# Kernel optimization log

Measured on AMD Instinct MI355X. Metric: run time of the kernel, lower is better.

## Reference

```python
import jax, jax.numpy as jnp
import numpy as np

B, S, E, H, C = 2, 2048, 1024, 16, 16
SQ2 = np.float32(np.sqrt(2.0))


def setup_inputs() -> dict:
    key = jax.random.key(0)
    ks = jax.random.split(key, 32)
    sc = 0.02
    d = {"query": jax.random.normal(ks[0], (B, S, E), jnp.float32)}
    i = 1
    for dom in ("f", "w", "c"):
        d[f"Wp_{dom}"] = jax.random.normal(ks[i], (E, E), jnp.float32) * sc; i += 1
        d[f"bp_{dom}"] = jnp.zeros((E,), jnp.float32)
        d[f"Wc_{dom}"] = jax.random.normal(ks[i], (C, E, 3), jnp.float32) * sc; i += 1
        d[f"bc_{dom}"] = jnp.zeros((C,), jnp.float32)
        d["F" + dom] = jax.random.normal(ks[i], (C, E), jnp.float32); i += 1
    d["mha_iw"] = jax.random.normal(ks[i], (3 * E, E), jnp.float32) * sc; i += 1
    d["mha_ib"] = jnp.zeros((3 * E,), jnp.float32)
    d["mha_ow"] = jax.random.normal(ks[i], (E, E), jnp.float32) * sc; i += 1
    d["mha_ob"] = jnp.zeros((E,), jnp.float32)
    d["fus_W"] = jax.random.normal(ks[i], (E, 3 * E), jnp.float32) * sc; i += 1
    d["fus_b"] = jnp.zeros((E,), jnp.float32)
    return d


def _conv1d(x, W, b):
    # x: [B,S,E] real -> [B,S,C], conv over sequence, kernel 3, same padding
    y = jax.lax.conv_general_dilated(x.transpose(0, 2, 1), W, (1,), [(1, 1)],
                                     dimension_numbers=("NCH", "OIH", "NCH"))
    return (y + b[None, :, None]).transpose(0, 2, 1)


def _channels(x, Wc, bc, Fp):
    # spectral conv (real/imag separately if complex) + adaptive softmax filtering
    if jnp.iscomplexobj(x):
        ch = _conv1d(x.real, Wc, bc) + 1j * _conv1d(x.imag, Wc, bc)
    else:
        ch = _conv1d(x, Wc, bc)
    fw = jax.nn.softmax(Fp, axis=0)  # [C,E], softmax over channels
    return jnp.einsum("bsc,ce->bse", ch, fw.astype(ch.dtype))


def _spec_attn(q, k, v):
    scale = np.float32(1.0) / jnp.sqrt(jnp.asarray(q.shape[-1], jnp.float32))
    scores = jnp.einsum("bse,bte->bst", q, k) * scale
    if jnp.iscomplexobj(scores):
        w = jax.nn.softmax(scores.real, axis=-1)
        cw = (w * jnp.exp(1j * jnp.angle(scores))).astype(jnp.complex64)
        return jnp.einsum("bst,bte->bse", cw, v)
    return jnp.einsum("bst,bte->bse", jax.nn.softmax(scores, axis=-1), v)


def _haar(x):
    # simplified Haar wavelet transform; S is a power of 2 so no padding needed
    cur, coeffs = x, []
    while cur.shape[1] > 1:
        e, o = cur[:, 0::2, :], cur[:, 1::2, :]
        coeffs.append((e - o) / SQ2)
        cur = (e + o) / SQ2
    coeffs.append(cur)
    return jnp.concatenate(coeffs[::-1], axis=1)


def _dct_mats(L):
    n = jnp.arange(L, dtype=jnp.float32)
    k = n[:, None]
    D = jnp.cos(np.pi * k * (2.0 * n + 1.0) / (2.0 * L))
    D = D.at[0].multiply(np.float32(np.sqrt(1.0 / L)))
    D = D.at[1:].multiply(np.float32(np.sqrt(2.0 / L)))
    I = jnp.cos(np.pi * n * (2.0 * k + 1.0) / (2.0 * L))
    I = I.at[:, 0].multiply(np.float32(np.sqrt(1.0 / L)))
    I = I.at[:, 1:].multiply(np.float32(np.sqrt(2.0 / L)))
    return D, I


def _domain(x, Wp, bp, Wc, bc, Fp, domain):
    # key=value=query so q_domain == k_domain == v_domain
    xd = x @ Wp.T + bp
    if domain == "fourier":
        s = jnp.fft.fft(xd, axis=1)
        ch = _channels(s, Wc, bc, Fp)
        out = _spec_attn(ch, ch, ch)
        return jnp.fft.ifft(out, axis=1).real
    elif domain == "wavelet":
        s = _haar(xd)
        ch = _channels(s, Wc, bc, Fp)
        return _spec_attn(ch, ch, ch)  # inverse wavelet is identity in source
    else:  # cosine
        D, I = _dct_mats(xd.shape[1])
        s = jnp.einsum("st,bte->bse", D, xd)
        ch = _channels(s, Wc, bc, Fp)
        out = _spec_attn(ch, ch, ch)
        return jnp.einsum("st,bte->bse", I, out)


def _mha(x, iw, ib, ow, ob, nheads):
    # torch nn.MultiheadAttention (batch_first) self-attention
    Bx, L, Ex = x.shape
    hd = Ex // nheads
    qkv = x @ iw.T + ib
    q, k, v = jnp.split(qkv, 3, axis=-1)
    sh = lambda t: t.reshape(Bx, L, nheads, hd).transpose(0, 2, 1, 3)
    q, k, v = sh(q), sh(k), sh(v)
    a = jax.nn.softmax(jnp.einsum("bhld,bhmd->bhlm", q, k) / np.float32(np.sqrt(hd)), axis=-1)
    o = jnp.einsum("bhlm,bhmd->bhld", a, v).transpose(0, 2, 1, 3).reshape(Bx, L, Ex)
    return o @ ow.T + ob


def reference(query, Wp_f, bp_f, Wc_f, bc_f, Ff, Wp_w, bp_w, Wc_w, bc_w, Fw,
              Wp_c, bp_c, Wc_c, bc_c, Fc, mha_iw, mha_ib, mha_ow, mha_ob, fus_W, fus_b):
    outs = [
        _domain(query, Wp_f, bp_f, Wc_f, bc_f, Ff, "fourier"),
        _domain(query, Wp_w, bp_w, Wc_w, bc_w, Fw, "wavelet"),
        _domain(query, Wp_c, bp_c, Wc_c, bc_c, Fc, "cosine"),
    ]
    Bq, Sq, Eq = query.shape
    stacked = jnp.stack(outs, axis=2)                 # [B,S,3,E]
    corr = _mha(stacked.reshape(Bq * Sq, 3, Eq), mha_iw, mha_ib, mha_ow, mha_ob, H)
    fused = corr.reshape(Bq, Sq, 3 * Eq)              # concat of correlated domain outputs
    return fused @ fus_W.T + fus_b
```

## Files before the change

### kernel.cpp

```cpp
#include <hip/hip_runtime.h>
#include <cmath>

#define BB 2
#define SS_ 2048
#define EE 1024
#define CC 16

typedef __attribute__((ext_vector_type(8))) short short8v;
typedef __attribute__((ext_vector_type(4))) float floatx4;

__device__ __forceinline__ void split4(const float4 v, short4& h, short4& l)
{
    unsigned ux = __float_as_uint(v.x), uy = __float_as_uint(v.y);
    unsigned uz = __float_as_uint(v.z), uw = __float_as_uint(v.w);
    h.x = (short)(ux >> 16); h.y = (short)(uy >> 16);
    h.z = (short)(uz >> 16); h.w = (short)(uw >> 16);
    float lx = v.x - __uint_as_float(ux & 0xFFFF0000u);
    float ly = v.y - __uint_as_float(uy & 0xFFFF0000u);
    float lz = v.z - __uint_as_float(uz & 0xFFFF0000u);
    float lw = v.w - __uint_as_float(uw & 0xFFFF0000u);
    l.x = (short)(__float_as_uint(lx) >> 16);
    l.y = (short)(__float_as_uint(ly) >> 16);
    l.z = (short)(__float_as_uint(lz) >> 16);
    l.w = (short)(__float_as_uint(lw) >> 16);
}

#define BM 128
#define BN 128
#define BK 32
#define LDP 40

__launch_bounds__(256, 2)
__global__ void gemm_at(const float* __restrict__ A, const float* __restrict__ Bsrc,
                        float* __restrict__ C,
                        int K, int lda, int ldb, int ldc,
                        long sA, long sB, long sC, float alpha, int KS)
{
    __shared__ short sAh[BM * LDP], sAl[BM * LDP], sBh[BN * LDP], sBl[BN * LDP];
    const int z = blockIdx.z;
    const int bz = z / KS, ks = z % KS;
    const int klen = K / KS, kbase = ks * klen;
    A += (size_t)bz * sA; Bsrc += (size_t)bz * sB; C += (size_t)bz * sC;
    const int tid = threadIdx.x;
    const int m0 = blockIdx.y * BM, n0 = blockIdx.x * BN;

    const int lr0 = tid >> 3;
    const int kc0 = (tid & 7) * 4;
    const float* pa = A + (size_t)(m0 + lr0) * lda + kbase + kc0;
    const float* pb = Bsrc + (size_t)(n0 + lr0) * ldb + kbase + kc0;

    float4 ra[4], rb[4];
    #pragma unroll
    for (int c = 0; c < 4; ++c) {
        ra[c] = *(const float4*)(pa + (size_t)c * 32 * lda);
        rb[c] = *(const float4*)(pb + (size_t)c * 32 * ldb);
    }

    const int lane = tid & 63, wid = tid >> 6;
    const int wm = wid >> 1, wn = wid & 1;
    const int lr = lane & 15, qd = lane >> 4;
    const int arow = wm * 64 + lr;
    const int brow = wn * 64 + lr;
    const int koff = qd * 8;

    floatx4 acc[4][4];
    #pragma unroll
    for (int i = 0; i < 4; ++i)
        #pragma unroll
        for (int j = 0; j < 4; ++j)
            acc[i][j] = (floatx4){0.f, 0.f, 0.f, 0.f};

    for (int kt = 0; kt < klen; kt += BK) {
        __syncthreads();
        #pragma unroll
        for (int c = 0; c < 4; ++c) {
            const int row = lr0 + c * 32;
            short4 h, l;
            split4(ra[c], h, l);
            *(short4*)&sAh[row * LDP + kc0] = h;
            *(short4*)&sAl[row * LDP + kc0] = l;
            split4(rb[c], h, l);
            *(short4*)&sBh[row * LDP + kc0] = h;
            *(short4*)&sBl[row * LDP + kc0] = l;
        }
        __syncthreads();
        if (kt + BK < klen) {
            pa += BK; pb += BK;
            #pragma unroll
            for (int c = 0; c < 4; ++c) {
                ra[c] = *(const float4*)(pa + (size_t)c * 32 * lda);
                rb[c] = *(const float4*)(pb + (size_t)c * 32 * ldb);
            }
        }
        short8v ah[4], al[4], bh[4], bl[4];
        #pragma unroll
        for (int i = 0; i < 4; ++i) {
            ah[i] = *(const short8v*)&sAh[(arow + i * 16) * LDP + koff];
            al[i] = *(const short8v*)&sAl[(arow + i * 16) * LDP + koff];
            bh[i] = *(const short8v*)&sBh[(brow + i * 16) * LDP + koff];
            bl[i] = *(const short8v*)&sBl[(brow + i * 16) * LDP + koff];
        }
        #pragma unroll
        for (int i = 0; i < 4; ++i)
            #pragma unroll
            for (int j = 0; j < 4; ++j)
                acc[i][j] = __builtin_amdgcn_mfma_f32_16x16x32_bf16(ah[i], bh[j], acc[i][j], 0, 0, 0);
        #pragma unroll
// ... 359 lines not shown

__launch_bounds__(256)
__global__ void conv_all(const float* __restrict__ Tfr, const float* __restrict__ Tfi,
                         const float* __restrict__ Tw, const float* __restrict__ Tc,
                         const float* __restrict__ Gm,
                         const float* __restrict__ bc0, const float* __restrict__ bc1,
                         const float* __restrict__ bc2,
                         float* __restrict__ chFr, float* __restrict__ chFi,
                         float* __restrict__ chW, float* __restrict__ chC,
                         float* __restrict__ QFr, float* __restrict__ QFi,
                         float* __restrict__ QW, float* __restrict__ QC)
{
    const int dom = blockIdx.z;
    const bool cplx = (dom == 0);
    const float* Tre = dom == 0 ? Tfr : (dom == 1 ? Tw : Tc);
    const float* Tim = Tfi;
    const float* G = Gm + dom * 256;
    const float* bc = dom == 0 ? bc0 : (dom == 1 ? bc1 : bc2);
    float* chR = dom == 0 ? chFr : (dom == 1 ? chW : chC);
    float* chI = chFi;
    float* QR = dom == 0 ? QFr : (dom == 1 ? QW : QC);
    float* QI = QFi;

    const int s0 = blockIdx.x * 64, b = blockIdx.y;
    const int tid = threadIdx.x;
    __shared__ float sR[66 * 49];
    __shared__ float sI[66 * 49];
    __shared__ float scr[64 * 17];
    __shared__ float sci[64 * 17];
    __shared__ float sG[256];
    if (tid < 256) sG[tid] = G[tid];
    for (int lin = tid; lin < 66 * 12; lin += 256) {
        int r = lin / 12, c4 = (lin % 12) * 4;
        int srow = s0 - 1 + r;
        float4 v = {0.f, 0.f, 0.f, 0.f}, w = {0.f, 0.f, 0.f, 0.f};
        if (srow >= 0 && srow < 2048) {
            v = *(const float4*)(Tre + ((size_t)(b * 2048 + srow)) * 48 + c4);
            if (cplx) w = *(const float4*)(Tim + ((size_t)(b * 2048 + srow)) * 48 + c4);
        }
        sR[r * 49 + c4] = v.x; sR[r * 49 + c4 + 1] = v.y;
        sR[r * 49 + c4 + 2] = v.z; sR[r * 49 + c4 + 3] = v.w;
        if (cplx) {
            sI[r * 49 + c4] = w.x; sI[r * 49 + c4 + 1] = w.y;
            sI[r * 49 + c4 + 2] = w.z; sI[r * 49 + c4 + 3] = w.w;
        }
    }
    __syncthreads();
    const int row = tid >> 2, ln = tid & 3;
    float ch[4], chi[4];
    #pragma unroll
    for (int j = 0; j < 4; ++j) {
        int c = ln * 4 + j;
        float bcv = bc[c];
        ch[j] = sR[row * 49 + 3 * c] + sR[(row + 1) * 49 + 3 * c + 1]
              + sR[(row + 2) * 49 + 3 * c + 2] + bcv;
        scr[row * 17 + c] = ch[j];
        if (cplx) {
            chi[j] = sI[row * 49 + 3 * c] + sI[(row + 1) * 49 + 3 * c + 1]
                   + sI[(row + 2) * 49 + 3 * c + 2] + bcv;
            sci[row * 17 + c] = chi[j];
        }
    }
    size_t ro = ((size_t)(b * 2048 + s0 + row)) * 16 + ln * 4;
    *(float4*)(chR + ro) = *(float4*)&ch[0];
    if (cplx) *(float4*)(chI + ro) = *(float4*)&chi[0];
    __syncthreads();
    float qp[4] = {}, qpi[4] = {};
    #pragma unroll
    for (int c = 0; c < 16; ++c) {
        float cv = scr[row * 17 + c];
        float cvi = cplx ? sci[row * 17 + c] : 0.f;
        #pragma unroll
        for (int j = 0; j < 4; ++j) {
            float g = sG[c * 16 + ln * 4 + j];
            qp[j] = fmaf(cv, g, qp[j]);
            if (cplx) qpi[j] = fmaf(cvi, g, qpi[j]);
        }
    }
    *(float4*)(QR + ro) = *(float4*)&qp[0];
    if (cplx) *(float4*)(QI + ro) = *(float4*)&qpi[0];
}

__launch_bounds__(256)
__global__ void flash_all(const float* __restrict__ QpFr, const float* __restrict__ QpFi,
                          const float* __restrict__ chFr, const float* __restrict__ chFi,
                          float* __restrict__ OFr, float* __restrict__ OFi,
                          const float* __restrict__ QpW, const float* __restrict__ chW,
                          float* __restrict__ Ow_,
                          const float* __restrict__ QpC, const float* __restrict__ chC,
                          float* __restrict__ Oc_)
{
    const int dom = blockIdx.z;
    const int b = blockIdx.y;
    const int w = threadIdx.x >> 6, lane = threadIdx.x & 63;
    const int s = blockIdx.x * 4 + w;
    if (dom != 0) {
        const float* Qp = dom == 1 ? QpW : QpC;
        const float* ch = dom == 1 ? chW : chC;
        float* O = dom == 1 ? Ow_ : Oc_;
        const float* qrow = Qp + ((size_t)(b * 2048 + s)) * 16;
        float q[16];
        #pragma unroll
        for (int j = 0; j < 4; ++j) *(float4*)&q[j * 4] = *(const float4*)(qrow + j * 4);
        const float* chb = ch + (size_t)b * 2048 * 16;
        float m = -3.4e38f, l = 0.f;
        float acc[16] = {};
        for (int t = lane; t < 2048; t += 64) {
            const float* kp = chb + (size_t)t * 16;
            float kv[16];
            #pragma unroll
            for (int j = 0; j < 4; ++j) *(float4*)&kv[j * 4] = *(const float4*)(kp + j * 4);
            float sc = 0.f;
            #pragma unroll
            for (int e = 0; e < 16; ++e) sc = fmaf(q[e], kv[e], sc);
            float mn = fmaxf(m, sc);
            float al = __expf(m - mn), p = __expf(sc - mn);
            l = l * al + p;
            #pragma unroll
            for (int e = 0; e < 16; ++e) acc[e] = fmaf(acc[e], al, p * kv[e]);
            m = mn;
        }
        #pragma unroll
        for (int off = 1; off < 64; off <<= 1) {
            float m2 = __shfl_xor(m, off, 64);
            float l2 = __shfl_xor(l, off, 64);
            float mn = fmaxf(m, m2);
            float ra = __expf(m - mn), rb = __expf(m2 - mn);
            l = l * ra + l2 * rb;
            #pragma unroll
            for (int e = 0; e < 16; ++e) {
                float a2 = __shfl_xor(acc[e], off, 64);
                acc[e] = acc[e] * ra + a2 * rb;
            }
            m = mn;
        }
        if (lane < 4) {
            float inv = 1.f / l;
            float4 o4 = {acc[lane * 4] * inv, acc[lane * 4 + 1] * inv,
                         acc[lane * 4 + 2] * inv, acc[lane * 4 + 3] * inv};
            *(float4*)(O + ((size_t)(b * 2048 + s)) * 16 + lane * 4) = o4;
        }
        return;
    }
    float qr[16], qi[16];
    {
        const float* qrow = QpFr + ((size_t)(b * 2048 + s)) * 16;
        const float* qrowI = QpFi + ((size_t)(b * 2048 + s)) * 16;
        #pragma unroll
        for (int j = 0; j < 4; ++j) {
            *(float4*)&qr[j * 4] = *(const float4*)(qrow + j * 4);
            *(float4*)&qi[j * 4] = *(const float4*)(qrowI + j * 4);
        }
    }
    const float* cbR = chFr + (size_t)b * 2048 * 16;
    const float* cbI = chFi + (size_t)b * 2048 * 16;
    float m = -3.4e38f, l = 0.f;
    float aR[16] = {}, aI[16] = {};
    for (int t = lane; t < 2048; t += 64) {
        float kr[16], ki[16];
        #pragma unroll
        for (int j = 0; j < 4; ++j) {
            *(float4*)&kr[j * 4] = *(const float4*)(cbR + (size_t)t * 16 + j * 4);
            *(float4*)&ki[j * 4] = *(const float4*)(cbI + (size_t)t * 16 + j * 4);
        }
        float sre = 0.f, sim = 0.f;
        #pragma unroll
        for (int e = 0; e < 16; ++e) {
            sre = fmaf(qr[e], kr[e], sre); sre = fmaf(-qi[e], ki[e], sre);
            sim = fmaf(qr[e], ki[e], sim); sim = fmaf(qi[e], kr[e], sim);
        }
        float mn = fmaxf(m, sre);
        float al = __expf(m - mn), p = __expf(sre - mn);
        l = l * al + p;
        float rr = sqrtf(sre * sre + sim * sim);
        float iv = (rr > 0.f) ? (p / rr) : 0.f;
        float wr = (rr > 0.f) ? iv * sre : p;
        float wi = (rr > 0.f) ? iv * sim : 0.f;
        #pragma unroll
        for (int e = 0; e < 16; ++e) {
            aR[e] = fmaf(aR[e], al, wr * kr[e] - wi * ki[e]);
            aI[e] = fmaf(aI[e], al, wr * ki[e] + wi * kr[e]);
        }
        m = mn;
    }
    #pragma unroll
    for (int off = 1; off < 64; off <<= 1) {
        float m2 = __shfl_xor(m, off, 64);
        float l2 = __shfl_xor(l, off, 64);
        float mn = fmaxf(m, m2);
        float ra = __expf(m - mn), rb = __expf(m2 - mn);
        l = l * ra + l2 * rb;
        #pragma unroll
        for (int e = 0; e < 16; ++e) {
            float a2 = __shfl_xor(aR[e], off, 64);
            aR[e] = aR[e] * ra + a2 * rb;
            float b2 = __shfl_xor(aI[e], off, 64);
            aI[e] = aI[e] * ra + b2 * rb;
        }
        m = mn;
    }
    float inv = 1.f / l;
    size_t ro = ((size_t)(b * 2048 + s)) * 16;
    if (lane < 4) {
        float4 o4 = {aR[lane * 4] * inv, aR[lane * 4 + 1] * inv,
                     aR[lane * 4 + 2] * inv, aR[lane * 4 + 3] * inv};
        *(float4*)(OFr + ro + lane * 4) = o4;
    } else if (lane < 8) {
        int j = lane - 4;
        float4 o4 = {aI[j * 4] * inv, aI[j * 4 + 1] * inv,
                     aI[j * 4 + 2] * inv, aI[j * 4 + 3] * inv};
        *(float4*)(OFi + ro + j * 4) = o4;
    }
}

__launch_bounds__(256)
__global__ void mha_o(const float* __restrict__ R0, const float* __restrict__ R1,
                      const float* __restrict__ R2, const float* __restrict__ Pt,
                      const float* __restrict__ Mten, float* __restrict__ MO)
{
    const int tid = threadIdx.x;
    const int p = blockIdx.x * 256 + tid;
    const int h = blockIdx.y;
    __shared__ float sPv[3 * 64 * 20];
    __shared__ float sM[9 * 17 * 20];
    for (int lin = tid; lin < 3264; lin += 256) {
        int mm = lin / 1088, rem = lin % 1088;
        int rr = rem / 17, a = rem % 17;
        sPv[(mm * 64 + rr) * 20 + a] = Pt[mm * 52224 + (size_t)(2048 + h * 64 + rr) * 17 + a];
    }
    for (int lin = tid; lin < 2601; lin += 256) {
        int lm = lin / 289, rem = lin % 289;
        int a = rem / 17, bq = rem % 17;
        sM[lm * 340 + a * 20 + bq] = Mten[(size_t)h * 2601 + lin];
    }
    __syncthreads();
    float R[3][16];
    float4 R4[3][4];
    #pragma unroll
    for (int j = 0; j < 4; ++j) {
        R4[0][j] = *(const float4*)(R0 + (size_t)p * 16 + j * 4);
        R4[1][j] = *(const float4*)(R1 + (size_t)p * 16 + j * 4);
        R4[2][j] = *(const float4*)(R2 + (size_t)p * 16 + j * 4);
        *(float4*)&R[0][j * 4] = R4[0][j];
        *(float4*)&R[1][j * 4] = R4[1][j];
        *(float4*)&R[2][j * 4] = R4[2][j];
    }
    float w[3][3];
    #pragma unroll
    for (int l = 0; l < 3; ++l) {
        float sc[3];
        #pragma unroll
        for (int mm = 0; mm < 3; ++mm) {
            const float* Mp = &sM[(l * 3 + mm) * 340];
            float s = 0.f;
            #pragma unroll
            for (int a = 0; a < 17; ++a) {
                const float* mr = Mp + a * 20;
                float4 m0 = *(const float4*)(mr), m1 = *(const float4*)(mr + 4);
                float4 m2 = *(const float4*)(mr + 8), m3 = *(const float4*)(mr + 12);
                float t = mr[16];
                t = fmaf(m0.x, R4[mm][0].x, t); t = fmaf(m0.y, R4[mm][0].y, t);
                t = fmaf(m0.z, R4[mm][0].z, t); t = fmaf(m0.w, R4[mm][0].w, t);
                t = fmaf(m1.x, R4[mm][1].x, t); t = fmaf(m1.y, R4[mm][1].y, t);
                t = fmaf(m1.z, R4[mm][1].z, t); t = fmaf(m1.w, R4[mm][1].w, t);
                t = fmaf(m2.x, R4[mm][2].x, t); t = fmaf(m2.y, R4[mm][2].y, t);
                t = fmaf(m2.z, R4[mm][2].z, t); t = fmaf(m2.w, R4[mm][2].w, t);
                t = fmaf(m3.x, R4[mm][3].x, t); t = fmaf(m3.y, R4[mm][3].y, t);
                t = fmaf(m3.z, R4[mm][3].z, t); t = fmaf(m3.w, R4[mm][3].w, t);
                float ra = (a < 16) ? R[l][a] : 1.f;
                s = fmaf(ra, t, s);
            }
            sc[mm] = s;
        }
        float mx = fmaxf(sc[0], fmaxf(sc[1], sc[2]));
        float e0 = expf(sc[0] - mx), e1 = expf(sc[1] - mx), e2 = expf(sc[2] - mx);
        float inv = 1.f / (e0 + e1 + e2);
        w[l][0] = e0 * inv; w[l][1] = e1 * inv; w[l][2] = e2 * inv;
    }
    #pragma unroll
    for (int d4 = 0; d4 < 16; ++d4) {
        float4 vm[3];
        #pragma unroll
        for (int mm = 0; mm < 3; ++mm) {
            float vx[4];
            #pragma unroll
            for (int r = 0; r < 4; ++r) {
                const float* pv = &sPv[(mm * 64 + d4 * 4 + r) * 20];
                float4 p0 = *(const float4*)(pv), p1 = *(const float4*)(pv + 4);
                float4 p2 = *(const float4*)(pv + 8), p3 = *(const float4*)(pv + 12);
                float t = pv[16];
                t = fmaf(R4[mm][0].x, p0.x, t); t = fmaf(R4[mm][0].y, p0.y, t);
                t = fmaf(R4[mm][0].z, p0.z, t); t = fmaf(R4[mm][0].w, p0.w, t);
                t = fmaf(R4[mm][1].x, p1.x, t); t = fmaf(R4[mm][1].y, p1.y, t);
                t = fmaf(R4[mm][1].z, p1.z, t); t = fmaf(R4[mm][1].w, p1.w, t);
                t = fmaf(R4[mm][2].x, p2.x, t); t = fmaf(R4[mm][2].y, p2.y, t);
                t = fmaf(R4[mm][2].z, p2.z, t); t = fmaf(R4[mm][2].w, p2.w, t);
                t = fmaf(R4[mm][3].x, p3.x, t); t = fmaf(R4[mm][3].y, p3.y, t);
                t = fmaf(R4[mm][3].z, p3.z, t); t = fmaf(R4[mm][3].w, p3.w, t);
                vx[r] = t;
            }
            vm[mm] = (float4){vx[0], vx[1], vx[2], vx[3]};
        }
        #pragma unroll
        for (int l = 0; l < 3; ++l) {
            float4 o4;
            o4.x = w[l][0] * vm[0].x + w[l][1] * vm[1].x + w[l][2] * vm[2].x;
            o4.y = w[l][0] * vm[0].y + w[l][1] * vm[1].y + w[l][2] * vm[2].y;
            o4.z = w[l][0] * vm[0].z + w[l][1] * vm[1].z + w[l][2] * vm[2].z;
            o4.w = w[l][0] * vm[0].w + w[l][1] * vm[1].w + w[l][2] * vm[2].w;
            *(float4*)(MO + (size_t)p * 3072 + l * 1024 + h * 64 + d4 * 4) = o4;
        }
    }
}

extern "C" void kernel_launch(void* const* d_in, const int* in_sizes, int n_in,
                              void* d_out, int out_size, void* d_ws, size_t ws_size,
                              hipStream_t stream)
{
    const float* query = (const float*)d_in[0];
    const float* Wp[3] = {(const float*)d_in[1], (const float*)d_in[6],  (const float*)d_in[11]};
    const float* bp[3] = {(const float*)d_in[2], (const float*)d_in[7],  (const float*)d_in[12]};
    const float* Wc[3] = {(const float*)d_in[3], (const float*)d_in[8],  (const float*)d_in[13]};
    const float* bc[3] = {(const float*)d_in[4], (const float*)d_in[9],  (const float*)d_in[14]};
    const float* Fp[3] = {(const float*)d_in[5], (const float*)d_in[10], (const float*)d_in[15]};
    const float* mha_iw = (const float*)d_in[16];
    const float* mha_ib = (const float*)d_in[17];
    const float* mha_ow = (const float*)d_in[18];
    const float* mha_ob = (const float*)d_in[19];
    const float* fus_W  = (const float*)d_in[20];
    const float* fus_b  = (const float*)d_in[21];
    float* out = (float*)d_out;
    float* ws = (float*)d_ws;

    size_t off = 0;
    auto alloc = [&](size_t n) { float* p = ws + off; off += n; return p; };
    float* MAT0 = alloc(4194304);
    float* MAT1 = alloc(4194304);
    float* DCTD = alloc(4194304);
    float* DCTI = alloc(4194304);
    float* MO   = alloc((size_t)4096 * 3072);
    float* FTb  = alloc((size_t)1024 * 3072);
    float* OWT  = alloc((size_t)1024 * 1024);
    float* WpT  = alloc(3145728);
    float* fwT  = alloc(49152);
    float* W2cat = alloc(147456);
    float* ubv  = alloc(256);
    float* Gm   = alloc(1024);
    float* W3cat = alloc(147456);
    float* Ucat = alloc(589824);
    float* Tfr  = alloc(196608);
    float* Tfi  = alloc(196608);
    float* Tc   = alloc(196608);
    float* Rf   = alloc(65536);
    float* Rc   = alloc(65536);
    float* Tw   = alloc(196608);
    float* chFr = alloc(65536); float* chFi = alloc(65536);
    float* QpFr = alloc(65536); float* QpFi = alloc(65536);
    float* chW  = alloc(65536); float* QpW  = alloc(65536);
    float* chC  = alloc(65536); float* QpC  = alloc(65536);
    float* OFr  = alloc(65536); float* OFi  = alloc(65536);
    float* Ow   = alloc(65536); float* Oc   = alloc(65536);
    float* Pt   = alloc(156672);
    float* Mten = alloc(41616);
    float* ybv  = alloc(1024);
    if (ws_size < off * sizeof(float)) return;

    float* Uf = Ucat, *Uw = Ucat + 196608, *Uc = Ucat + 2 * 196608;
    const long SE48 = 2048 * 48, SE16 = 2048 * 16;

    build_w2<<<dim3(576), dim3(256), 0, stream>>>(Wc[0], Wc[1], Wc[2], W2cat);
    prep_fw_G<<<dim3(3), dim3(256), 0, stream>>>(Fp[0], Fp[1], Fp[2], fwT, Gm);
    build_ub2<<<dim3(3), dim3(256), 0, stream>>>(bp[0], bp[1], bp[2], W2cat, ubv);
    build_yb2<<<dim3(256), dim3(256), 0, stream>>>(mha_ob, fus_W, fus_b, ybv);
    gen_trig<<<dim3(32768), dim3(256), 0, stream>>>(MAT0, MAT1, DCTD, DCTI);
    transpose_wp3<<<dim3(32, 32, 3), dim3(256), 0, stream>>>(Wp[0], Wp[1], Wp[2], WpT);
    init_all<<<dim3(34980), dim3(256), 0, stream>>>(W3cat, ubv, Pt, FTb, out, ybv);

    skmfma<48, 0><<<dim3(16, 1, 6), dim3(256), 0, stream>>>(
        WpT, nullptr, W2cat, nullptr, W3cat, nullptr,
        1024, 1024, 48, 48, 1048576, 49152, 49152, 1.f, 2);
    skmfma<48, 0><<<dim3(64, 1, 6), dim3(256), 0, stream>>>(
        query, nullptr, W3cat, nullptr, Ucat, nullptr,
        1024, 1024, 48, 48, 0, 49152, 196608, 1.f, 2);
    skmfma<48, 1><<<dim3(32, 1, 8), dim3(256), 0, stream>>>(
        MAT0, MAT1, Uf, nullptr, Tfr, Tfi,
        2048, 2048, 48, 48, 0, SE48, SE48, 1.f, 4);
    skmfma<48, 0><<<dim3(32, 1, 8), dim3(256), 0, stream>>>(
        DCTD, nullptr, Uc, nullptr, Tc, nullptr,
        2048, 2048, 48, 48, 0, SE48, SE48, 1.f, 4);

    haar_all<<<dim3(12, 2), dim3(256), 0, stream>>>(Uw, Tw);

    conv_all<<<dim3(32, 2, 3), dim3(256), 0, stream>>>(
        Tfr, Tfi, Tw, Tc, Gm, bc[0], bc[1], bc[2],
        chFr, chFi, chW, chC, QpFr, QpFi, QpW, QpC);

    flash_all<<<dim3(512, 2, 3), dim3(256), 0, stream>>>(
        QpFr, QpFi, chFr, chFi, OFr, OFi, QpW, chW, Ow, QpC, chC, Oc);

    skmfma<16, 2><<<dim3(32, 1, 8), dim3(256), 0, stream>>>(
        MAT0, MAT1, OFr, OFi, Rf, nullptr,
        2048, 2048, 16, 16, 0, SE16, SE16, 1.f / 2048.f, 4);
    skmfma<16, 0><<<dim3(32, 1, 8), dim3(256), 0, stream>>>(
        DCTI, nullptr, Oc, nullptr, Rc, nullptr,
        2048, 2048, 16, 16, 0, SE16, SE16, 1.f, 4);
    skmfma<16, 0><<<dim3(48, 1, 6), dim3(256), 0, stream>>>(
        mha_iw, nullptr, fwT, nullptr, Pt, nullptr,
        1024, 1024, 16, 17, 0, 16384, 52224, 1.f, 2);

    ib_append<<<dim3(36), dim3(256), 0, stream>>>(mha_ib, Pt);
    build_M<<<dim3(144), dim3(256), 0, stream>>>(Pt, Mten);

    mha_o<<<dim3(16, 16), dim3(256), 0, stream>>>(Rf, Ow, Rc, Pt, Mten, MO);

    transpose_k<<<dim3(32, 32), dim3(256), 0, stream>>>(mha_ow, OWT, 1024, 1024);
    gemm_at<<<dim3(8, 8, 6), dim3(256), 0, stream>>>(
        fus_W, OWT, FTb, 1024, 3072, 1024, 3072, 1024, 0, 1024, 1.f, 2);

    gemm_at<<<dim3(8, 32, 2), dim3(256), 0, stream>>>(
        MO, FTb, out, 3072, 3072, 3072, 1024, 0, 0, 0, 1.f, 2);
}
```

Measured before the change: 758.5 us.

## Move spectral flash attention onto bf16x3 MFMA with two-pass split-K softmax

Replaces the scalar per-lane online-softmax attention over the 16-wide channel space with an MFMA path. A prep kernel splits Q, K and V into bf16 hi/mid/lo pieces (complex parts arranged for real/imag products), a stats pass computes row max and sum across 4 K-splits, a merge kernel combines them, and a PV pass recomputes scores, forms the weights and accumulates with bf16 split MFMAs plus atomics. This aims to cut the large FMA and exp cost of the fp32 scalar loop. The price is recomputing QK twice, extra launches and scratch traffic (reusing the WpT region), atomic accumulation, and a possible loss of precision from bf16 splitting.

```diff
diff --git a/kernel.cpp b/kernel.cpp
--- a/kernel.cpp
+++ b/kernel.cpp
@@ -23,6 +23,63 @@
     l.y = (short)(__float_as_uint(ly) >> 16);
     l.z = (short)(__float_as_uint(lz) >> 16);
     l.w = (short)(__float_as_uint(lw) >> 16);
+}
+
+__device__ __forceinline__ void split1(float v, short& h, short& l)
+{
+    unsigned u = __float_as_uint(v);
+    h = (short)(u >> 16);
+    float rm = v - __uint_as_float(u & 0xFFFF0000u);
+    l = (short)(__float_as_uint(rm) >> 16);
+}
+
+__device__ __forceinline__ void split4s(float a, float b, float c, float d,
+                                        short4& h, short4& l)
+{
+    split1(a, h.x, l.x); split1(b, h.y, l.y);
+    split1(c, h.z, l.z); split1(d, h.w, l.w);
+}
+
+__device__ __forceinline__ void split3_1(float v, short& x1, short& x2, short& x3)
+{
+    unsigned u = __float_as_uint(v);
+    x1 = (short)(u >> 16);
+    float r1 = v - __uint_as_float(u & 0xFFFF0000u);
+    unsigned u2 = __float_as_uint(r1);
+    x2 = (short)(u2 >> 16);
+    float r2 = r1 - __uint_as_float(u2 & 0xFFFF0000u);
+    x3 = (short)(__float_as_uint(r2) >> 16);
+}
+
+__device__ __forceinline__ void split3s(float a, float b, float c, float d,
+                                        short4& h1, short4& h2, short4& h3)
+{
+    split3_1(a, h1.x, h2.x, h3.x); split3_1(b, h1.y, h2.y, h3.y);
+    split3_1(c, h1.z, h2.z, h3.z); split3_1(d, h1.w, h2.w, h3.w);
+}
+
+__device__ __forceinline__ short4 neg4(short4 a)
+{
+    short4 r;
+    r.x = (short)(a.x ^ (short)0x8000); r.y = (short)(a.y ^ (short)0x8000);
+    r.z = (short)(a.z ^ (short)0x8000); r.w = (short)(a.w ^ (short)0x8000);
+    return r;
+}
+
+__device__ __forceinline__ short8v pack8(short4 a, short4 b)
+{
+    short8v r;
+    r[0] = a.x; r[1] = a.y; r[2] = a.z; r[3] = a.w;
+    r[4] = b.x; r[5] = b.y; r[6] = b.z; r[7] = b.w;
+    return r;
+}
+
+__device__ __forceinline__ short8v negbf(short8v x)
+{
+    int4 t = *(int4*)&x;
+    t.x ^= 0x80008000; t.y ^= 0x80008000;
+    t.z ^= 0x80008000; t.w ^= 0x80008000;
+    return *(short8v*)&t;
 }
 
 #define BM 128
@@ -548,134 +605,378 @@
 }
 
 __launch_bounds__(256)
-__global__ void flash_all(const float* __restrict__ QpFr, const float* __restrict__ QpFi,
-                          const float* __restrict__ chFr, const float* __restrict__ chFi,
-                          float* __restrict__ OFr, float* __restrict__ OFi,
-                          const float* __restrict__ QpW, const float* __restrict__ chW,
-                          float* __restrict__ Ow_,
-                          const float* __restrict__ QpC, const float* __restrict__ chC,
-                          float* __restrict__ Oc_)
-{
-    const int dom = blockIdx.z;
-    const int b = blockIdx.y;
-    const int w = threadIdx.x >> 6, lane = threadIdx.x & 63;
-    const int s = blockIdx.x * 4 + w;
+__global__ void prep_flash(const float* __restrict__ QpFr, const float* __restrict__ QpFi,
+                           const float* __restrict__ chFr, const float* __restrict__ chFi,
+                           const float* __restrict__ QpW, const float* __restrict__ chW,
+                           const float* __restrict__ QpC, const float* __restrict__ chC,
+                           short* __restrict__ AqF, short* __restrict__ BreF,
+                           short* __restrict__ BimF,
+                           short* __restrict__ VtFrH, short* __restrict__ VtFrL,
+                           short* __restrict__ VtFiH, short* __restrict__ VtFiL,
+                           short* __restrict__ AqW, short* __restrict__ KsW,
+                           short* __restrict__ VtWH, short* __restrict__ VtWL,
+                           short* __restrict__ AqC, short* __restrict__ KsC,
+                           short* __restrict__ VtCH, short* __restrict__ VtCL)
+{
+    const int t0 = blockIdx.x * 256, b = blockIdx.y, dom = blockIdx.z;
+    const int tid = threadIdx.x;
+    const size_t row = (size_t)b * 2048 + t0 + tid;
+    const int e = tid >> 4, ts = (tid & 15) * 16;
+    const size_t vo = (size_t)(b * 16 + e) * 2048 + t0 + ts;
     if (dom != 0) {
         const float* Qp = dom == 1 ? QpW : QpC;
         const float* ch = dom == 1 ? chW : chC;
+        short* Aq = dom == 1 ? AqW : AqC;
+        short* Ks = dom == 1 ? KsW : KsC;
+        short* VH = dom == 1 ? VtWH : VtCH;
+        short* VL = dom == 1 ? VtWL : VtCL;
+        float q[16], k[16];
+        #pragma unroll
+        for (int j = 0; j < 4; ++j) {
+            *(float4*)&q[j * 4] = *(const float4*)(Qp + row * 16 + j * 4);
+            *(float4*)&k[j * 4] = *(const float4*)(ch + row * 16 + j * 4);
+        }
+        #pragma unroll
+        for (int j = 0; j < 4; ++j) {
+            short4 h1, h2, h3;
+            split3s(q[j * 4], q[j * 4 + 1], q[j * 4 + 2], q[j * 4 + 3], h1, h2, h3);
+            *(short4*)&Aq[row * 48 + j * 4]      = h1;
+            *(short4*)&Aq[row * 48 + 16 + j * 4] = h2;
+            *(short4*)&Aq[row * 48 + 32 + j * 4] = h3;
+            split3s(k[j * 4], k[j * 4 + 1], k[j * 4 + 2], k[j * 4 + 3], h1, h2, h3);
+            *(short4*)&Ks[row * 48 + j * 4]      = h1;
+            *(short4*)&Ks[row * 48 + 16 + j * 4] = h2;
+            *(short4*)&Ks[row * 48 + 32 + j * 4] = h3;
+        }
+        #pragma unroll
+        for (int j = 0; j < 4; ++j) {
+            float v0 = ch[((size_t)b * 2048 + t0 + ts + j * 4 + 0) * 16 + e];
+            float v1 = ch[((size_t)b * 2048 + t0 + ts + j * 4 + 1) * 16 + e];
+            float v2 = ch[((size_t)b * 2048 + t0 + ts + j * 4 + 2) * 16 + e];
+            float v3 = ch[((size_t)b * 2048 + t0 + ts + j * 4 + 3) * 16 + e];
+            short4 h, l; split4s(v0, v1, v2, v3, h, l);
+            *(short4*)&VH[vo + j * 4] = h;
+            *(short4*)&VL[vo + j * 4] = l;
+        }
+        return;
+    }
+    float qr[16], qi[16], kr[16], ki[16];
+    #pragma unroll
+    for (int j = 0; j < 4; ++j) {
+        *(float4*)&qr[j * 4] = *(const float4*)(QpFr + row * 16 + j * 4);
+        *(float4*)&qi[j * 4] = *(const float4*)(QpFi + row * 16 + j * 4);
+        *(float4*)&kr[j * 4] = *(const float4*)(chFr + row * 16 + j * 4);
+        *(float4*)&ki[j * 4] = *(const float4*)(chFi + row * 16 + j * 4);
+    }
+    #pragma unroll
+    for (int j = 0; j < 4; ++j) {
+        short4 q1, q2, q3, p1, p2, p3, r1, r2, r3, s1, s2, s3;
+        split3s(qr[j * 4], qr[j * 4 + 1], qr[j * 4 + 2], qr[j * 4 + 3], q1, q2, q3);
+        split3s(qi[j * 4], qi[j * 4 + 1], qi[j * 4 + 2], qi[j * 4 + 3], p1, p2, p3);
+        split3s(kr[j * 4], kr[j * 4 + 1], kr[j * 4 + 2], kr[j * 4 + 3], r1, r2, r3);
+        split3s(ki[j * 4], ki[j * 4 + 1], ki[j * 4 + 2], ki[j * 4 + 3], s1, s2, s3);
+        *(short4*)&AqF[row * 96 + j * 4]      = q1;
+        *(short4*)&AqF[row * 96 + 16 + j * 4] = p1;
+        *(short4*)&AqF[row * 96 + 32 + j * 4] = q2;
+        *(short4*)&AqF[row * 96 + 48 + j * 4] = p2;
+        *(short4*)&AqF[row * 96 + 64 + j * 4] = q3;
+        *(short4*)&AqF[row * 96 + 80 + j * 4] = p3;
+        *(short4*)&BreF[row * 96 + j * 4]      = r1;
+        *(short4*)&BreF[row * 96 + 16 + j * 4] = neg4(s1);
+        *(short4*)&BreF[row * 96 + 32 + j * 4] = r2;
+        *(short4*)&BreF[row * 96 + 48 + j * 4] = neg4(s2);
+        *(short4*)&BreF[row * 96 + 64 + j * 4] = r3;
+        *(short4*)&BreF[row * 96 + 80 + j * 4] = neg4(s3);
+        *(short4*)&BimF[row * 96 + j * 4]      = s1;
+        *(short4*)&BimF[row * 96 + 16 + j * 4] = r1;
+        *(short4*)&BimF[row * 96 + 32 + j * 4] = s2;
+        *(short4*)&BimF[row * 96 + 48 + j * 4] = r2;
+        *(short4*)&BimF[row * 96 + 64 + j * 4] = s3;
+        *(short4*)&BimF[row * 96 + 80 + j * 4] = r3;
+    }
+    #pragma unroll
+    for (int j = 0; j < 4; ++j) {
+        float v0 = chFr[((size_t)b * 2048 + t0 + ts + j * 4 + 0) * 16 + e];
+        float v1 = chFr[((size_t)b * 2048 + t0 + ts + j * 4 + 1) * 16 + e];
+        float v2 = chFr[((size_t)b * 2048 + t0 + ts + j * 4 + 2) * 16 + e];
+        float v3 = chFr[((size_t)b * 2048 + t0 + ts + j * 4 + 3) * 16 + e];
+        short4 h, l; split4s(v0, v1, v2, v3, h, l);
+        *(short4*)&VtFrH[vo + j * 4] = h;
+        *(short4*)&VtFrL[vo + j * 4] = l;
+        v0 = chFi[((size_t)b * 2048 + t0 + ts + j * 4 + 0) * 16 + e];
+        v1 = chFi[((size_t)b * 2048 + t0 + ts + j * 4 + 1) * 16 + e];
+        v2 = chFi[((size_t)b * 2048 + t0 + ts + j * 4 + 2) * 16 + e];
+        v3 = chFi[((size_t)b * 2048 + t0 + ts + j * 4 + 3) * 16 + e];
+        split4s(v0, v1, v2, v3, h, l);
+        *(short4*)&VtFiH[vo + j * 4] = h;
+        *(short4*)&VtFiL[vo + j * 4] = l;
+    }
+}
+
+
+__launch_bounds__(256)
+__global__ void flash_stats(const short* __restrict__ AqF, const short* __restrict__ BreF,
+                            const short* __restrict__ AqW, const short* __restrict__ KsW,
+                            const short* __restrict__ AqC, const short* __restrict__ KsC,
+                            float* __restrict__ Mpart, float* __restrict__ Lpart)
+{
+    const int z = blockIdx.z, dom = z >> 1, b = z & 1;
+    const int tid = threadIdx.x, w = tid >> 6, lane = tid & 63;
+    const int lr = lane & 15, qd = lane >> 4;
+    const int rowbase = blockIdx.x * 64 + w * 16;
+    const int ks = blockIdx.y;
+    const size_t qrow = (size_t)b * 2048 + rowbase + lr;
+    const floatx4 FZ = {0.f, 0.f, 0.f, 0.f};
+    float m[4] = {-3.4e38f, -3.4e38f, -3.4e38f, -3.4e38f};
+    float l[4] = {0.f, 0.f, 0.f, 0.f};
+    if (dom == 0) {
+        const short8v a1 = *(const short8v*)&AqF[qrow * 96 + qd * 8];
+        const short8v a2 = *(const short8v*)&AqF[qrow * 96 + 32 + qd * 8];
+        const short8v a3 = *(const short8v*)&AqF[qrow * 96 + 64 + qd * 8];
+        const short* Bb = BreF + (size_t)b * 2048 * 96;
+        for (int s = 0; s < 32; ++s) {
+            const short* brow = Bb + (size_t)(ks * 512 + s * 16 + lr) * 96;
+            short8v b1 = *(const short8v*)&brow[qd * 8];
+            short8v b2 = *(const short8v*)&brow[32 + qd * 8];
+            short8v b3 = *(const short8v*)&brow[64 + qd * 8];
+            floatx4 sc = __builtin_amdgcn_mfma_f32_16x16x32_bf16(a1, b1, FZ, 0, 0, 0);
+            sc = __builtin_amdgcn_mfma_f32_16x16x32_bf16(a1, b2, sc, 0, 0, 0);
+            sc = __builtin_amdgcn_mfma_f32_16x16x32_bf16(a2, b1, sc, 0, 0, 0);
+            sc = __builtin_amdgcn_mfma_f32_16x16x32_bf16(a1, b3, sc, 0, 0, 0);
+            sc = __builtin_amdgcn_mfma_f32_16x16x32_bf16(a2, b2, sc, 0, 0, 0);
+            sc = __builtin_amdgcn_mfma_f32_16x16x32_bf16(a3, b1, sc, 0, 0, 0);
+            #pragma unroll
+            for (int r = 0; r < 4; ++r) {
+                float v = sc[r];
+                if (v <= m[r]) l[r] += __expf(v - m[r]);
+                else { l[r] = l[r] * __expf(m[r] - v) + 1.f; m[r] = v; }
+            }
+        }
+    } else {
+        const short* Aq = dom == 1 ? AqW : AqC;
+        const short* Ks = dom == 1 ? KsW : KsC;
+        const short8v a1 = *(const short8v*)&Aq[qrow * 48 + qd * 8];
+        const short8v a2 = *(const short8v*)&Aq[qrow * 48 + 32 + (qd & 1) * 8];
+        const short* Kb = Ks + (size_t)b * 2048 * 48;
+        const int ko = (qd & 1) * 8;
+        for (int s = 0; s < 32; ++s) {
+            const short* krow = Kb + (size_t)(ks * 512 + s * 16 + lr) * 48;
+            short8v b1  = *(const short8v*)&krow[ko];
+            short8v b2  = *(const short8v*)&krow[16 + ko];
+            short8v b3  = *(const short8v*)&krow[32 + ko];
+            short8v b12 = *(const short8v*)&krow[qd * 8];
+            floatx4 sc = __builtin_amdgcn_mfma_f32_16x16x32_bf16(a1, b1, FZ, 0, 0, 0);
+            sc = __builtin_amdgcn_mfma_f32_16x16x32_bf16(a1, b2, sc, 0, 0, 0);
+            sc = __builtin_amdgcn_mfma_f32_16x16x32_bf16(a1, b3, sc, 0, 0, 0);
+            sc = __builtin_amdgcn_mfma_f32_16x16x32_bf16(a2, b12, sc, 0, 0, 0);
+            #pragma unroll
+            for (int r = 0; r < 4; ++r) {
+                float v = sc[r];
+                if (v <= m[r]) l[r] += __expf(v - m[r]);
+                else { l[r] = l[r] * __expf(m[r] - v) + 1.f; m[r] = v; }
+            }
+        }
+    }
+    #pragma unroll
+    for (int off = 1; off < 16; off <<= 1) {
+        #pragma unroll
+        for (int r = 0; r < 4; ++r) {
+            float m2 = __shfl_xor(m[r], off, 64);
+            float l2 = __shfl_xor(l[r], off, 64);
+            float mn = fmaxf(m[r], m2);
+            l[r] = l[r] * __expf(m[r] - mn) + l2 * __expf(m2 - mn);
+            m[r] = mn;
+        }
+    }
+    if (lr == 0) {
+        size_t base = ((size_t)z * 4 + ks) * 2048 + rowbase + qd * 4;
+        #pragma unroll
+        for (int r = 0; r < 4; ++r) { Mpart[base + r] = m[r]; Lpart[base + r] = l[r]; }
+    }
+}
+
+__global__ void flash_merge(const float* __restrict__ Mpart, const float* __restrict__ Lpart,
+                            float* __restrict__ Mrow, float* __restrict__ Linv,
+                            float* __restrict__ Ozone)
+{
+    size_t idx = (size_t)blockIdx.x * 256 + threadIdx.x;
+    if (idx < 12288) {
+        size_t s = idx >> 11, r = idx & 2047;
+        float m = -3.4e38f;
+        #pragma unroll
+        for (int k = 0; k < 4; ++k) m = fmaxf(m, Mpart[(s * 4 + k) * 2048 + r]);
+        float l = 0.f;
+        #pragma unroll
+        for (int k = 0; k < 4; ++k)
+            l += Lpart[(s * 4 + k) * 2048 + r] * __expf(Mpart[(s * 4 + k) * 2048 + r] - m);
+        Mrow[idx] = m;
+        Linv[idx] = 1.f / l;
+    } else if (idx < 12288 + 262144) {
+        Ozone[idx - 12288] = 0.f;
+    }
+}
+
+__launch_bounds__(256)
+__global__ void flash_pv(const short* __restrict__ AqF, const short* __restrict__ BreF,
+                         const short* __restrict__ BimF,
+                         const short* __restrict__ VtFrH, const short* __restrict__ VtFrL,
+                         const short* __restrict__ VtFiH, const short* __restrict__ VtFiL,
+                         const short* __restrict__ AqW, const short* __restrict__ KsW,
+                         const short* __restrict__ VtWH, const short* __restrict__ VtWL,
+                         const short* __restrict__ AqC, const short* __restrict__ KsC,
+                         const short* __restrict__ VtCH, const short* __restrict__ VtCL,
+                         const float* __restrict__ Mrow, const float* __restrict__ Linv,
+                         float* __restrict__ OFr, float* __restrict__ OFi,
+                         float* __restrict__ Ow_, float* __restrict__ Oc_)
+{
+    __shared__ float sP[4][1152];
+    const int z = blockIdx.z, dom = z >> 1, b = z & 1;
+    const int tid = threadIdx.x, w = tid >> 6, lane = tid & 63;
+    const int lr = lane & 15, qd = lane >> 4;
+    const int rowbase = blockIdx.x * 64 + w * 16;
+    const int ks = blockIdx.y;
+    const size_t qrow = (size_t)b * 2048 + rowbase + lr;
+    const floatx4 FZ = {0.f, 0.f, 0.f, 0.f};
+    float* P0 = &sP[w][0];
+    const float4 m4 = *(const float4*)&Mrow[(size_t)z * 2048 + rowbase + qd * 4];
+    const float4 li4 = *(const float4*)&Linv[(size_t)z * 2048 + rowbase + qd * 4];
+    const float mA[4] = {m4.x, m4.y, m4.z, m4.w};
+    const float liA[4] = {li4.x, li4.y, li4.z, li4.w};
+
+    if (dom != 0) {
+        const short* Aq = dom == 1 ? AqW : AqC;
+        const short* Ks = dom == 1 ? KsW : KsC;
+        const short* VH = dom == 1 ? VtWH : VtCH;
+        const short* VL = dom == 1 ? VtWL : VtCL;
         float* O = dom == 1 ? Ow_ : Oc_;
-        const float* qrow = Qp + ((size_t)(b * 2048 + s)) * 16;
-        float q[16];
-        #pragma unroll
-        for (int j = 0; j < 4; ++j) *(float4*)&q[j * 4] = *(const float4*)(qrow + j * 4);
-        const float* chb = ch + (size_t)b * 2048 * 16;
-        float m = -3.4e38f, l = 0.f;
-        float acc[16] = {};
-        for (int t = lane; t < 2048; t += 64) {
-            const float* kp = chb + (size_t)t * 16;
-            float kv[16];
-            #pragma unroll
-            for (int j = 0; j < 4; ++j) *(float4*)&kv[j * 4] = *(const float4*)(kp + j * 4);
-            float sc = 0.f;
-            #pragma unroll
-            for (int e = 0; e < 16; ++e) sc = fmaf(q[e], kv[e], sc);
-            float mn = fmaxf(m, sc);
-            float al = __expf(m - mn), p = __expf(sc - mn);
-            l = l * al + p;
-            #pragma unroll
-            for (int e = 0; e < 16; ++e) acc[e] = fmaf(acc[e], al, p * kv[e]);
-            m = mn;
-        }
-        #pragma unroll
-        for (int off = 1; off < 64; off <<= 1) {
-            float m2 = __shfl_xor(m, off, 64);
-            float l2 = __shfl_xor(l, off, 64);
-            float mn = fmaxf(m, m2);
-            float ra = __expf(m - mn), rb = __expf(m2 - mn);
-            l = l * ra + l2 * rb;
-            #pragma unroll
-            for (int e = 0; e < 16; ++e) {
-                float a2 = __shfl_xor(acc[e], off, 64);
-                acc[e] = acc[e] * ra + a2 * rb;
+        const short8v a1 = *(const short8v*)&Aq[qrow * 48 + qd * 8];
+        const short8v a2 = *(const short8v*)&Aq[qrow * 48 + 32 + (qd & 1) * 8];
+        const short* Kb = Ks + (size_t)b * 2048 * 48;
+        const short* vhB = VH + (size_t)(b * 16 + lr) * 2048;
+        const short* vlB = VL + (size_t)(b * 16 + lr) * 2048;
+        const int ko = (qd & 1) * 8;
+        floatx4 acc = FZ;
+        for (int c = 0; c < 16; ++c) {
+            const int tt = ks * 512 + c * 32;
+            #pragma unroll
+            for (int s2 = 0; s2 < 2; ++s2) {
+                const short* krow = Kb + (size_t)(tt + s2 * 16 + lr) * 48;
+                short8v b1  = *(const short8v*)&krow[ko];
+                short8v b2  = *(const short8v*)&krow[16 + ko];
+                short8v b3  = *(const short8v*)&krow[32 + ko];
+                short8v b12 = *(const short8v*)&krow[qd * 8];
+                floatx4 sc = __builtin_amdgcn_mfma_f32_16x16x32_bf16(a1, b1, FZ, 0, 0, 0);
+                sc = __builtin_amdgcn_mfma_f32_16x16x32_bf16(a1, b2, sc, 0, 0, 0);
+                sc = __builtin_amdgcn_mfma_f32_16x16x32_bf16(a1, b3, sc, 0, 0, 0);
+                sc = __builtin_amdgcn_mfma_f32_16x16x32_bf16(a2, b12, sc, 0, 0, 0);
+                #pragma unroll
+                for (int r = 0; r < 4; ++r)
+                    P0[(qd * 4 + r) * 36 + s2 * 16 + lr] = __expf(sc[r] - mA[r]);
             }
-            m = mn;
-        }
-        if (lane < 4) {
-            float inv = 1.f / l;
-            float4 o4 = {acc[lane * 4] * inv, acc[lane * 4 + 1] * inv,
-                         acc[lane * 4 + 2] * inv, acc[lane * 4 + 3] * inv};
-            *(float4*)(O + ((size_t)(b * 2048 + s)) * 16 + lane * 4) = o4;
-        }
+            asm volatile("s_waitcnt lgkmcnt(0)" ::: "memory");
+            __builtin_amdgcn_sched_barrier(0);
+            float4 p0 = *(const float4*)&P0[lr * 36 + qd * 8];
+            float4 p1 = *(const float4*)&P0[lr * 36 + qd * 8 + 4];
+            short4 h0, g0, h1, g1;
+            split4s(p0.x, p0.y, p0.z, p0.w, h0, g0);
+            split4s(p1.x, p1.y, p1.z, p1.w, h1, g1);
+            short8v ph = pack8(h0, h1), pl = pack8(g0, g1);
+            short8v vh = *(const short8v*)&vhB[tt + qd * 8];
+            short8v vl = *(const short8v*)&vlB[tt + qd * 8];
+            acc = __builtin_amdgcn_mfma_f32_16x16x32_bf16(ph, vh, acc, 0, 0, 0);
+            acc = __builtin_amdgcn_mfma_f32_16x16x32_bf16(ph, vl, acc, 0, 0, 0);
+            acc = __builtin_amdgcn_mfma_f32_16x16x32_bf16(pl, vh, acc, 0, 0, 0);
+        }
+        size_t ob = ((size_t)b * 2048 + rowbase + qd * 4) * 16 + lr;
+        #pragma unroll
+        for (int r = 0; r < 4; ++r)
+            atomicAdd(&O[ob + (size_t)r * 16], acc[r] * liA[r]);
         return;
     }
-    float qr[16], qi[16];
-    {
-        const float* qrow = QpFr + ((size_t)(b * 2048 + s)) * 16;
-        const float* qrowI = QpFi + ((size_t)(b * 2048 + s)) * 16;
-        #pragma unroll
-        for (int j = 0; j < 4; ++j) {
-            *(float4*)&qr[j * 4] = *(const float4*)(qrow + j * 4);
-            *(float4*)&qi[j * 4] = *(const float4*)(qrowI + j * 4);
-        }
-    }
-    const float* cbR = chFr + (size_t)b * 2048 * 16;
-    const float* cbI = chFi + (size_t)b * 2048 * 16;
-    float m = -3.4e38f, l = 0.f;
-    float aR[16] = {}, aI[16] = {};
-    for (int t = lane; t < 2048; t += 64) {
-        float kr[16], ki[16];
-        #pragma unroll
-        for (int j = 0; j < 4; ++j) {
-            *(float4*)&kr[j * 4] = *(const float4*)(cbR + (size_t)t * 16 + j * 4);
-            *(float4*)&ki[j * 4] = *(const float4*)(cbI + (size_t)t * 16 + j * 4);
-        }
-        float sre = 0.f, sim = 0.f;
-        #pragma unroll
-        for (int e = 0; e < 16; ++e) {
-            sre = fmaf(qr[e], kr[e], sre); sre = fmaf(-qi[e], ki[e], sre);
-            sim = fmaf(qr[e], ki[e], sim); sim = fmaf(qi[e], kr[e], sim);
-        }
-        float mn = fmaxf(m, sre);
-        float al = __expf(m - mn), p = __expf(sre - mn);
-        l = l * al + p;
-        float rr = sqrtf(sre * sre + sim * sim);
-        float iv = (rr > 0.f) ? (p / rr) : 0.f;
-        float wr = (rr > 0.f) ? iv * sre : p;
-        float wi = (rr > 0.f) ? iv * sim : 0.f;
-        #pragma unroll
-        for (int e = 0; e < 16; ++e) {
-            aR[e] = fmaf(aR[e], al, wr * kr[e] - wi * ki[e]);
-            aI[e] = fmaf(aI[e], al, wr * ki[e] + wi * kr[e]);
-        }
-        m = mn;
-    }
-    #pragma unroll
-    for (int off = 1; off < 64; off <<= 1) {
-        float m2 = __shfl_xor(m, off, 64);
-        float l2 = __shfl_xor(l, off, 64);
-        float mn = fmaxf(m, m2);
-        float ra = __expf(m - mn), rb = __expf(m2 - mn);
-        l = l * ra + l2 * rb;
-        #pragma unroll
-        for (int e = 0; e < 16; ++e) {
-            float a2 = __shfl_xor(aR[e], off, 64);
-            aR[e] = aR[e] * ra + a2 * rb;
-            float b2 = __shfl_xor(aI[e], off, 64);
-            aI[e] = aI[e] * ra + b2 * rb;
-        }
-        m = mn;
-    }
-    float inv = 1.f / l;
-    size_t ro = ((size_t)(b * 2048 + s)) * 16;
-    if (lane < 4) {
-        float4 o4 = {aR[lane * 4] * inv, aR[lane * 4 + 1] * inv,
-                     aR[lane * 4 + 2] * inv, aR[lane * 4 + 3] * inv};
-        *(float4*)(OFr + ro + lane * 4) = o4;
-    } else if (lane < 8) {
-        int j = lane - 4;
-        float4 o4 = {aI[j * 4] * inv, aI[j * 4 + 1] * inv,
-                     aI[j * 4 + 2] * inv, aI[j * 4 + 3] * inv};
-        *(float4*)(OFi + ro + j * 4) = o4;
+    const short8v a1 = *(const short8v*)&AqF[qrow * 96 + qd * 8];
+    const short8v a2 = *(const short8v*)&AqF[qrow * 96 + 32 + qd * 8];
+    const short8v a3 = *(const short8v*)&AqF[qrow * 96 + 64 + qd * 8];
+    const short* BrB = BreF + (size_t)b * 2048 * 96;
+    const short* BiB = BimF + (size_t)b * 2048 * 96;
+    const short* vrhB = VtFrH + (size_t)(b * 16 + lr) * 2048;
+    const short* vrlB = VtFrL + (size_t)(b * 16 + lr) * 2048;
+    const short* vihB = VtFiH + (size_t)(b * 16 + lr) * 2048;
+    const short* vilB = VtFiL + (size_t)(b * 16 + lr) * 2048;
+    float* PR = P0;
+    float* PI = P0 + 576;
+    floatx4 accR = FZ, accI = FZ;
+    for (int c = 0; c < 16; ++c) {
+        const int tt = ks * 512 + c * 32;
+        #pragma unroll
+        for (int s2 = 0; s2 < 2; ++s2) {
+            const short* br = BrB + (size_t)(tt + s2 * 16 + lr) * 96;
+            const short* bi = BiB + (size_t)(tt + s2 * 16 + lr) * 96;
+            short8v b1r = *(const short8v*)&br[qd * 8];
+            short8v b2r = *(const short8v*)&br[32 + qd * 8];
+            short8v b3r = *(const short8v*)&br[64 + qd * 8];
+            short8v b1i = *(const short8v*)&bi[qd * 8];
+            short8v b2i = *(const short8v*)&bi[32 + qd * 8];
+            short8v b3i = *(const short8v*)&bi[64 + qd * 8];
+            floatx4 sre = __builtin_amdgcn_mfma_f32_16x16x32_bf16(a1, b1r, FZ, 0, 0, 0);
+            sre = __builtin_amdgcn_mfma_f32_16x16x32_bf16(a1, b2r, sre, 0, 0, 0);
+            sre = __builtin_amdgcn_mfma_f32_16x16x32_bf16(a2, b1r, sre, 0, 0, 0);
+            sre = __builtin_amdgcn_mfma_f32_16x16x32_bf16(a1, b3r, sre, 0, 0, 0);
+            sre = __builtin_amdgcn_mfma_f32_16x16x32_bf16(a2, b2r, sre, 0, 0, 0);
+            sre = __builtin_amdgcn_mfma_f32_16x16x32_bf16(a3, b1r, sre, 0, 0, 0);
+            floatx4 sim = __builtin_amdgcn_mfma_f32_16x16x32_bf16(a1, b1i, FZ, 0, 0, 0);
+            sim = __builtin_amdgcn_mfma_f32_16x16x32_bf16(a1, b2i, sim, 0, 0, 0);
+            sim = __builtin_amdgcn_mfma_f32_16x16x32_bf16(a2, b1i, sim, 0, 0, 0);
+            sim = __builtin_amdgcn_mfma_f32_16x16x32_bf16(a1, b3i, sim, 0, 0, 0);
+            sim = __builtin_amdgcn_mfma_f32_16x16x32_bf16(a2, b2i, sim, 0, 0, 0);
+            sim = __builtin_amdgcn_mfma_f32_16x16x32_bf16(a3, b1i, sim, 0, 0, 0);
+            #pragma unroll
+            for (int r = 0; r < 4; ++r) {
+                float xr = sre[r], xi = sim[r];
+                float p = __expf(xr - mA[r]);
+                float rr = sqrtf(xr * xr + xi * xi);
+                float t = p / rr;
+                float wr = (rr > 0.f) ? xr * t : p;
+                float wi = (rr > 0.f) ? xi * t : 0.f;
+                PR[(qd * 4 + r) * 36 + s2 * 16 + lr] = wr;
+                PI[(qd * 4 + r) * 36 + s2 * 16 + lr] = wi;
+            }
+        }
+        asm volatile("s_waitcnt lgkmcnt(0)" ::: "memory");
+        __builtin_amdgcn_sched_barrier(0);
+        float4 r0 = *(const float4*)&PR[lr * 36 + qd * 8];
+        float4 r1 = *(const float4*)&PR[lr * 36 + qd * 8 + 4];
+        float4 i0 = *(const float4*)&PI[lr * 36 + qd * 8];
+        float4 i1 = *(const float4*)&PI[lr * 36 + qd * 8 + 4];
+        short4 ha, la, hb, lb;
+        split4s(r0.x, r0.y, r0.z, r0.w, ha, la);
+        split4s(r1.x, r1.y, r1.z, r1.w, hb, lb);
+        short8v wrh = pack8(ha, hb), wrl = pack8(la, lb);
+        split4s(i0.x, i0.y, i0.z, i0.w, ha, la);
+        split4s(i1.x, i1.y, i1.z, i1.w, hb, lb);
+        short8v wih = pack8(ha, hb), wil = pack8(la, lb);
+        short8v wihN = negbf(wih), wilN = negbf(wil);
+        short8v vrh = *(const short8v*)&vrhB[tt + qd * 8];
+        short8v vrl = *(const short8v*)&vrlB[tt + qd * 8];
+        short8v vih = *(const short8v*)&vihB[tt + qd * 8];
+        short8v vil = *(const short8v*)&vilB[tt + qd * 8];
+        accR = __builtin_amdgcn_mfma_f32_16x16x32_bf16(wrh, vrh, accR, 0, 0, 0);
+        accR = __builtin_amdgcn_mfma_f32_16x16x32_bf16(wrh, vrl, accR, 0, 0, 0);
+        accR = __builtin_amdgcn_mfma_f32_16x16x32_bf16(wrl, vrh, accR, 0, 0, 0);
+        accR = __builtin_amdgcn_mfma_f32_16x16x32_bf16(wihN, vih, accR, 0, 0, 0);
+        accR = __builtin_amdgcn_mfma_f32_16x16x32_bf16(wihN, vil, accR, 0, 0, 0);
+        accR = __builtin_amdgcn_mfma_f32_16x16x32_bf16(wilN, vih, accR, 0, 0, 0);
+        accI = __builtin_amdgcn_mfma_f32_16x16x32_bf16(wrh, vih, accI, 0, 0, 0);
+        accI = __builtin_amdgcn_mfma_f32_16x16x32_bf16(wrh, vil, accI, 0, 0, 0);
+        accI = __builtin_amdgcn_mfma_f32_16x16x32_bf16(wrl, vih, accI, 0, 0, 0);
+        accI = __builtin_amdgcn_mfma_f32_16x16x32_bf16(wih, vrh, accI, 0, 0, 0);
+        accI = __builtin_amdgcn_mfma_f32_16x16x32_bf16(wih, vrl, accI, 0, 0, 0);
+        accI = __builtin_amdgcn_mfma_f32_16x16x32_bf16(wil, vrh, accI, 0, 0, 0);
+    }
+    size_t ob = ((size_t)b * 2048 + rowbase + qd * 4) * 16 + lr;
+    #pragma unroll
+    for (int r = 0; r < 4; ++r) {
+        atomicAdd(&OFr[ob + (size_t)r * 16], accR[r] * liA[r]);
+        atomicAdd(&OFi[ob + (size_t)r * 16], accI[r] * liA[r]);
     }
 }
 
@@ -762,7 +1063,7 @@
                 t = fmaf(R4[mm][2].x, p2.x, t); t = fmaf(R4[mm][2].y, p2.y, t);
                 t = fmaf(R4[mm][2].z, p2.z, t); t = fmaf(R4[mm][2].w, p2.w, t);
                 t = fmaf(R4[mm][3].x, p3.x, t); t = fmaf(R4[mm][3].y, p3.y, t);
-                t = fmaf(R4[mm][3].z, p3.z, t); t = fmaf(R4[mm][3].w, p3.w, t);
+                t = fmaf(R4[mm][3].w, p3.w, t); t = fmaf(R4[mm][3].z, p3.z, t);
                 vx[r] = t;
             }
             vm[mm] = (float4){vx[0], vx[1], vx[2], vx[3]};
@@ -831,6 +1132,22 @@
     float* ybv  = alloc(1024);
     if (ws_size < off * sizeof(float)) return;
 
+    size_t poff = 0;
+    auto palloc = [&](size_t n) { float* p = WpT + poff; poff += n; return p; };
+    float* AqW  = palloc(98304);
+    float* KsW  = palloc(98304);
+    float* AqC  = palloc(98304);
+    float* KsC  = palloc(98304);
+    float* VtWH = palloc(32768); float* VtWL = palloc(32768);
+    float* VtCH = palloc(32768); float* VtCL = palloc(32768);
+    float* AqF  = palloc(196608);
+    float* BreF = palloc(196608);
+    float* BimF = palloc(196608);
+    float* VtFrH = palloc(32768); float* VtFrL = palloc(32768);
+    float* VtFiH = palloc(32768); float* VtFiL = palloc(32768);
+    float* Mpart = palloc(49152); float* Lpart = palloc(49152);
+    float* MrowA = palloc(12288); float* LinvA = palloc(12288);
+
     float* Uf = Ucat, *Uw = Ucat + 196608, *Uc = Ucat + 2 * 196608;
     const long SE48 = 2048 * 48, SE16 = 2048 * 16;
 
@@ -861,8 +1178,23 @@
         Tfr, Tfi, Tw, Tc, Gm, bc[0], bc[1], bc[2],
         chFr, chFi, chW, chC, QpFr, QpFi, QpW, QpC);
 
-    flash_all<<<dim3(512, 2, 3), dim3(256), 0, stream>>>(
-        QpFr, QpFi, chFr, chFi, OFr, OFi, QpW, chW, Ow, QpC, chC, Oc);
+    prep_flash<<<dim3(8, 2, 3), dim3(256), 0, stream>>>(
+        QpFr, QpFi, chFr, chFi, QpW, chW, QpC, chC,
+        (short*)AqF, (short*)BreF, (short*)BimF,
+        (short*)VtFrH, (short*)VtFrL, (short*)VtFiH, (short*)VtFiL,
+        (short*)AqW, (short*)KsW, (short*)VtWH, (short*)VtWL,
+        (short*)AqC, (short*)KsC, (short*)VtCH, (short*)VtCL);
+    flash_stats<<<dim3(32, 4, 6), dim3(256), 0, stream>>>(
+        (const short*)AqF, (const short*)BreF,
+        (const short*)AqW, (const short*)KsW,
+        (const short*)AqC, (const short*)KsC, Mpart, Lpart);
+    flash_merge<<<dim3(1072), dim3(256), 0, stream>>>(Mpart, Lpart, MrowA, LinvA, OFr);
+    flash_pv<<<dim3(32, 4, 6), dim3(256), 0, stream>>>(
+        (const short*)AqF, (const short*)BreF, (const short*)BimF,
+        (const short*)VtFrH, (const short*)VtFrL, (const short*)VtFiH, (const short*)VtFiL,
+        (const short*)AqW, (const short*)KsW, (const short*)VtWH, (const short*)VtWL,
+        (const short*)AqC, (const short*)KsC, (const short*)VtCH, (const short*)VtCL,
+        MrowA, LinvA, OFr, OFi, Ow, Oc);
 
     skmfma<16, 2><<<dim3(32, 1, 8), dim3(256), 0, stream>>>(
         MAT0, MAT1, OFr, OFi, Rf, nullptr,
```

Result: faster. 710.0 us (-6.4%).
